# Performance work log

Hardware: AMD Instinct MI355X
Metric: run time of the kernel (lower is better)

Reference implementation:

```python
import jax, jax.numpy as jnp
import numpy as np

B, C, H, W = 8, 512, 64, 64
K = 19       # num classes (Cityscapes)
CT = 256     # transform channels


def _proj(x, w, g, b):
    # 1x1 conv (no bias) + folded eval-mode BatchNorm (per-channel scale g, bias b) + ReLU
    # x: [B,Cin,H,W], w: [Cout,Cin]
    y = jnp.einsum('bchw,oc->bohw', x, w)
    return jax.nn.relu(y * g[None, :, None, None] + b[None, :, None, None])


def setup_inputs() -> dict:
    key = jax.random.key(0)
    ks = jax.random.split(key, 12)
    s = lambda i, shape: jax.random.normal(ks[i], shape, jnp.float32) * 0.05
    ones = lambda n: jnp.ones((n,), jnp.float32)
    zeros = lambda n: jnp.zeros((n,), jnp.float32)
    return {
        'x': jax.random.normal(ks[0], (B, C, H, W), jnp.float32),
        'preds': jax.random.normal(ks[1], (B, K, H, W), jnp.float32),
        'feats_il': jax.random.normal(ks[2], (B, C, H, W), jnp.float32),
        # query_project: two 1x1 conv+BN+ReLU blocks
        'q_w1': s(3, (CT, C)), 'q_g1': ones(CT), 'q_b1': zeros(CT),
        'q_w2': s(4, (CT, CT)), 'q_g2': ones(CT), 'q_b2': zeros(CT),
        # key_project: two 1x1 conv+BN+ReLU blocks
        'k_w1': s(5, (CT, C)), 'k_g1': ones(CT), 'k_b1': zeros(CT),
        'k_w2': s(6, (CT, CT)), 'k_g2': ones(CT), 'k_b2': zeros(CT),
        # value_project: one 1x1 conv+BN+ReLU (value_out_norm=True)
        'v_w': s(7, (CT, C)), 'v_g': ones(CT), 'v_b': zeros(CT),
        # out_project: one 1x1 conv+BN+ReLU
        'o_w': s(8, (C, CT)), 'o_g': ones(C), 'o_b': zeros(C),
    }


def reference(x, preds, feats_il, q_w1, q_g1, q_b1, q_w2, q_g2, q_b2,
              k_w1, k_g1, k_b1, k_w2, k_g2, k_b2, v_w, v_g, v_b, o_w, o_g, o_b):
    b, c, h, w = x.shape
    k = preds.shape[1]
    hw = h * w
    feats = x.reshape(b, c, hw).transpose(0, 2, 1)        # [B,HW,C]
    logits = preds.reshape(b, k, hw).transpose(0, 2, 1)   # [B,HW,K]
    argmax = jnp.argmax(logits, axis=-1)                  # [B,HW]
    onehot = jax.nn.one_hot(argmax, k, dtype=x.dtype)     # [B,HW,K]
    NEG = jnp.asarray(-1e9, x.dtype)
    masked = jnp.where(onehot > 0, logits, NEG)
    # per-class softmax over the pixels assigned to that class
    wgt = jax.nn.softmax(masked, axis=1)                  # [B,HW,K]
    cls_feat = jnp.einsum('bpk,bpc->bkc', wgt, feats)     # [B,K,C]
    # scatter class descriptor back to every pixel of that class
    feats_sl = jnp.take_along_axis(cls_feat, argmax[:, :, None], axis=1)  # [B,HW,C]
    feats_sl = feats_sl.transpose(0, 2, 1).reshape(b, c, h, w)
    # SelfAttentionBlock: query from inputs, key/value from feats_sl
    q = _proj(_proj(x, q_w1, q_g1, q_b1), q_w2, q_g2, q_b2)
    kk = _proj(_proj(feats_sl, k_w1, k_g1, k_b1), k_w2, k_g2, k_b2)
    v = _proj(feats_sl, v_w, v_g, v_b)
    ct = q.shape[1]
    qf = q.reshape(b, ct, hw).transpose(0, 2, 1)          # [B,HW,CT]
    kf = kk.reshape(b, ct, hw)                            # [B,CT,HW]
    vf = v.reshape(b, ct, hw).transpose(0, 2, 1)          # [B,HW,CT]
    sim = jnp.einsum('bqc,bck->bqk', qf, kf) * (ct ** -0.5)
    attn = jax.nn.softmax(sim, axis=-1)
    ctx = jnp.einsum('bqk,bkc->bqc', attn, vf)            # [B,HW,CT]
    ctx = ctx.transpose(0, 2, 1).reshape(b, ct, h, w)
    return _proj(ctx, o_w, o_g, o_b)
```

## Files before the change

### kernel.cpp

```cpp
#include <hip/hip_runtime.h>
#include <math.h>

#define HW 4096
#define NB 8
#define NK 19
#define CIN 512
#define CTC 256

typedef __attribute__((ext_vector_type(8))) short short8;
typedef __attribute__((ext_vector_type(4))) float f32x4;

__device__ inline unsigned short f2bf(float x) {
  unsigned u = __float_as_uint(x);
  return (unsigned short)((u + 0x7fffu + ((u >> 16) & 1u)) >> 16);
}
__device__ inline float bf2f(unsigned short h) {
  return __uint_as_float(((unsigned)h) << 16);
}
__device__ inline void gload16(const void* g, void* l) {
  __builtin_amdgcn_global_load_lds(
      (const __attribute__((address_space(1))) void*)g,
      (__attribute__((address_space(3))) void*)l, 16, 0, 0);
}

__global__ __launch_bounds__(256) void wk1a(
    const float* __restrict__ w1, const float* __restrict__ w2,
    const float* __restrict__ wo, unsigned short* __restrict__ wb1,
    unsigned short* __restrict__ wb2, unsigned short* __restrict__ wbo,
    uint4* __restrict__ cls_feat_z, const float* __restrict__ preds,
    float* __restrict__ bestg, int* __restrict__ clsg,
    unsigned int* __restrict__ Mu_part, unsigned int* __restrict__ cnt_part) {
  __shared__ unsigned int Mw[NK];
  __shared__ unsigned int Cw[NK];
  int bx = blockIdx.x;
  int tid = threadIdx.x;
  if (bx < 320) {
    int gid = bx * 256 + tid;
    int i = gid * 4;
    const float* src;
    unsigned short* dst;
    int off;
    if (i < 131072) { src = w1; dst = wb1; off = i; }
    else if (i < 196608) { src = w2; dst = wb2; off = i - 131072; }
    else { src = wo; dst = wbo; off = i - 196608; }
    float4 v = *(const float4*)(src + off);
    dst[off + 0] = f2bf(v.x);
    dst[off + 1] = f2bf(v.y);
    dst[off + 2] = f2bf(v.z);
    dst[off + 3] = f2bf(v.w);
    uint4 z = {0u, 0u, 0u, 0u};
    for (int j = gid; j < 19456; j += 81920) cls_feat_z[j] = z;
  } else {
    int bq = bx - 320;
    int b = bq >> 4, pblk = bq & 15;
    if (tid < NK) { Mw[tid] = 0u; Cw[tid] = 0u; }
    __syncthreads();
    int p = pblk * 256 + tid;
    const float* pb = preds + (size_t)b * NK * HW;
    float best = pb[p];
    int bi = 0;
#pragma unroll
    for (int k = 1; k < NK; ++k) {
      float v = pb[k * HW + p];
      if (v > best) { best = v; bi = k; }
    }
    bestg[b * HW + p] = best;
    clsg[b * HW + p] = bi;
    unsigned fb = __float_as_uint(best);
    unsigned key = (fb & 0x80000000u) ? ~fb : (fb | 0x80000000u);
    atomicMax(&Mw[bi], key);
    atomicAdd(&Cw[bi], 1u);
    __syncthreads();
    if (tid < 32) {
      Mu_part[(b * 16 + pblk) * 32 + tid] = (tid < NK) ? Mw[tid] : 0u;
      cnt_part[(b * 16 + pblk) * 32 + tid] = (tid < NK) ? Cw[tid] : 0u;
    }
  }
}

__global__ __launch_bounds__(256) void k1b(
    float* __restrict__ bestg, const int* __restrict__ clsg,
    const unsigned int* __restrict__ Mu_part, float* __restrict__ Zf_part) {
  int b = blockIdx.y, pblk = blockIdx.x;
  int tid = threadIdx.x;
  __shared__ float Mf[NK];
  __shared__ float Zw[NK];
  if (tid < NK) {
    unsigned key = 0u;
#pragma unroll
    for (int j = 0; j < 16; ++j) {
      unsigned v = Mu_part[(b * 16 + j) * 32 + tid];
      key = (v > key) ? v : key;
    }
    float m = -1e30f;
    if (key) {
      unsigned fb = (key & 0x80000000u) ? (key & 0x7fffffffu) : ~key;
      m = __uint_as_float(fb);
    }
    Mf[tid] = m;
    Zw[tid] = 0.f;
  }
  __syncthreads();
  int p = pblk * 256 + tid;
  int c = clsg[b * HW + p];
  float e = expf(bestg[b * HW + p] - Mf[c]);
  bestg[b * HW + p] = e;
  atomicAdd(&Zw[c], e);
  __syncthreads();
  if (tid < 32) Zf_part[(b * 16 + pblk) * 32 + tid] = (tid < NK) ? Zw[tid] : 0.f;
}

__global__ __launch_bounds__(256) void xk2(
    const float* __restrict__ x, const float* __restrict__ eg,
    const int* __restrict__ clsg, const float* __restrict__ Zf_part,
    unsigned short* __restrict__ xT, float* __restrict__ cls_feat) {
  __shared__ float tile[64][65];
  __shared__ unsigned short Bs[32 * 516];
  __shared__ float Zl[NK];
  int b = blockIdx.z, c0 = blockIdx.y * 64, pbase = blockIdx.x * 512;
  int tid = threadIdx.x;
  int l = tid & 63, w = tid >> 6;
  if (tid < NK) {
    float s = 0.f;
#pragma unroll
    for (int j = 0; j < 16; ++j) s += Zf_part[(b * 16 + j) * 32 + tid];
    Zl[tid] = s;
  }
  {
    uint4 z = {0u, 0u, 0u, 0u};
    for (int i = tid; i < 2064; i += 256) ((uint4*)Bs)[i] = z;
  }
  __syncthreads();
  for (int i = tid; i < 512; i += 256) {
    int c = clsg[b * HW + pbase + i];
    Bs[c * 516 + i] = f2bf(eg[b * HW + pbase + i] / Zl[c]);
  }
  f32x4 acc[2];
  acc[0] = (f32x4){0.f, 0.f, 0.f, 0.f};
  acc[1] = (f32x4){0.f, 0.f, 0.f, 0.f};
  int cbase = w * 16;
  for (int s = 0; s < 8; ++s) {
    int ps = pbase + s * 64;
    __syncthreads();
#pragma unroll
    for (int r = 0; r < 4; ++r) {
      int cl = r * 16 + (tid >> 4);
      int pl = (tid & 15) * 4;
      float4 v = *(const float4*)&x[((size_t)b * CIN + c0 + cl) * HW + ps + pl];
      tile[cl][pl + 0] = v.x;
      tile[cl][pl + 1] = v.y;
      tile[cl][pl + 2] = v.z;
      tile[cl][pl + 3] = v.w;
    }
    __syncthreads();
#pragma unroll
    for (int j = 0; j < 16; ++j) {
      int ploc = j * 4 + w;
      xT[((size_t)b * HW + ps + ploc) * CIN + c0 + l] = f2bf(tile[l][ploc]);
    }
#pragma unroll
    for (int ch = 0; ch < 2; ++ch) {
      int pt = ch * 32 + (l >> 4) * 8;
      union { short8 v; unsigned short u[8]; } af;
      const float* tp = &tile[cbase + (l & 15)][pt];
#pragma unroll
      for (int j = 0; j < 8; ++j) af.u[j] = f2bf(tp[j]);
      int pg = s * 64 + pt;
#pragma unroll
      for (int mf = 0; mf < 2; ++mf) {
        short8 bf = *(const short8*)&Bs[(mf * 16 + (l & 15)) * 516 + pg];
        acc[mf] =
            __builtin_amdgcn_mfma_f32_16x16x32_bf16(af.v, bf, acc[mf], 0, 0, 0);
      }
    }
  }
#pragma unroll
  for (int mf = 0; mf < 2; ++mf) {
    int k = mf * 16 + (l & 15);
    if (k < NK) {
#pragma unroll
      for (int r = 0; r < 4; ++r) {
        int c = c0 + cbase + (l >> 4) * 4 + r;
        atomicAdd(&cls_feat[((size_t)b * NK + k) * CIN + c], acc[mf][r]);
      }
    }
  }
}

__global__ __launch_bounds__(256) void k3a(
    const float* __restrict__ cls_feat, const float* __restrict__ kw1,
    const float* __restrict__ kg1, const float* __restrict__ kb1,
    const float* __restrict__ vw, const float* __restrict__ vg,
    const float* __restrict__ vb, float* __restrict__ h1g,
    float* __restrict__ Vcls) {
  int bk = blockIdx.y;
  int b = bk / NK, kc = bk % NK;
  int q = blockIdx.x;
  __shared__ float cf[CIN];
  int tid = threadIdx.x;
  const float* row = cls_feat + (size_t)bk * CIN;
  for (int i = tid; i < CIN; i += 256) cf[i] = row[i];
  __syncthreads();
  int o = tid >> 1, half = tid & 1;
  int col = q * 64 + (o & 63);
  const float* w =
      (o < 64) ? &kw1[(size_t)col * CIN] : &vw[(size_t)col * CIN];
  int base = half * 256;
  float acc[4] = {0.f, 0.f, 0.f, 0.f};
#pragma unroll 8
  for (int i = 0; i < 64; ++i) {
    float4 w4 = *(const float4*)&w[base + i * 4];
    const float* c4 = &cf[base + i * 4];
    acc[i & 3] += w4.x * c4[0] + w4.y * c4[1] + w4.z * c4[2] + w4.w * c4[3];
  }
  float s = (acc[0] + acc[1]) + (acc[2] + acc[3]);
  s += __shfl_xor(s, 1);
  if (half == 0) {
    if (o < 64) {
      h1g[(size_t)bk * CTC + col] = fmaxf(s * kg1[col] + kb1[col], 0.f);
    } else {
      Vcls[((size_t)b * CTC + col) * NK + kc] =
          fmaxf(s * vg[col] + vb[col], 0.f);
    }
  }
}

__global__ __launch_bounds__(256) void k3b(
    const float* __restrict__ h1g, const float* __restrict__ kw2,
    const float* __restrict__ kg2, const float* __restrict__ kb2,
    unsigned short* __restrict__ KclsT) {
  int bk = blockIdx.y;
  int q = blockIdx.x;
  __shared__ float h1[CTC];
  int tid = threadIdx.x;
  const float* row = h1g + (size_t)bk * CTC;
  if (tid < CTC) h1[tid] = row[tid];
  __syncthreads();
  int o = tid >> 2, part = tid & 3;
  int col = q * 64 + o;
  const float* w = &kw2[(size_t)col * CTC + part * 64];
  const float* c = &h1[part * 64];
  float acc[4] = {0.f, 0.f, 0.f, 0.f};
#pragma unroll
  for (int i = 0; i < 16; ++i) {
    float4 w4 = *(const float4*)&w[i * 4];
    acc[i & 3] += w4.x * c[i * 4] + w4.y * c[i * 4 + 1] + w4.z * c[i * 4 + 2] +
                  w4.w * c[i * 4 + 3];
  }
  float s = (acc[0] + acc[1]) + (acc[2] + acc[3]);
  s += __shfl_xor(s, 1);
  s += __shfl_xor(s, 2);
  if (part == 0)
    KclsT[(size_t)bk * CTC + col] = f2bf(fmaxf(s * kg2[col] + kb2[col], 0.f));
}

template <int KD>
__global__ __launch_bounds__(256) void gemm_mfma(
    const unsigned short* __restrict__ A, const unsigned short* __restrict__ Wb,
    const float* __restrict__ g, const float* __restrict__ bb,
    void* __restrict__ Y, int M, int outmode) {
  __shared__ __align__(16) unsigned short As[2][128 * 32];
  __shared__ __align__(16) unsigned short Bs[2][128 * 32];
  int b = blockIdx.z;
  int n0 = blockIdx.x * 128;
  int m0 = blockIdx.y * 128;
  int tid = threadIdx.x;
  int l = tid & 63, wid = tid >> 6;
  int wr = wid >> 1, wc = wid & 1;
  const unsigned short* Ab = A + (size_t)b * HW * KD;

  f32x4 acc[4][4];
#pragma unroll
  for (int i = 0; i < 4; ++i)
#pragma unroll
    for (int j = 0; j < 4; ++j) acc[i][j] = (f32x4){0.f, 0.f, 0.f, 0.f};

  const int NT = KD / 32;
  auto STAGE = [&](int buf, int t) {
    int k0 = t * 32;
#pragma unroll
    for (int q = 0; q < 2; ++q) {
      int e = q * 2048 + tid * 8;
      int rl = e >> 5, sl = (e >> 3) & 3;
      gload16(Ab + (size_t)(n0 + rl) * KD + k0 + 8 * (sl ^ ((rl >> 1) & 3)),
              &As[buf][q * 2048 + wid * 512]);
    }
#pragma unroll
    for (int q = 0; q < 2; ++q) {
      int e = q * 2048 + tid * 8;
      int rl = e >> 5, sl = (e >> 3) & 3;
      gload16(Wb + (size_t)(m0 + rl) * KD + k0 + 8 * (sl ^ ((rl >> 1) & 3)),
              &Bs[buf][q * 2048 + wid * 512]);
    }
  };
  STAGE(0, 0);
  for (int t = 0; t < NT; ++t) {
    __syncthreads();
    if (t + 1 < NT) STAGE((t + 1) & 1, t + 1);
    int cur = t & 1;
    short8 af[4], bf[4];
#pragma unroll
    for (int f = 0; f < 4; ++f) {
      int nl = wr * 64 + f * 16 + (l & 15);
      af[f] = *(const short8*)&As[cur][nl * 32 + 8 * ((l >> 4) ^ ((nl >> 1) & 3))];
      int ml = wc * 64 + f * 16 + (l & 15);
      bf[f] = *(const short8*)&Bs[cur][ml * 32 + 8 * ((l >> 4) ^ ((ml >> 1) & 3))];
    }
#pragma unroll
    for (int i = 0; i < 4; ++i)
#pragma unroll
      for (int j = 0; j < 4; ++j)
        acc[i][j] =
            __builtin_amdgcn_mfma_f32_16x16x32_bf16(af[i], bf[j], acc[i][j], 0, 0, 0);
  }
  if (outmode == 0) {
    float* Yf = (float*)Y + (size_t)b * M * HW;
#pragma unroll
    for (int j = 0; j < 4; ++j) {
      int m = m0 + wc * 64 + j * 16 + (l & 15);
      float gm = g[m], bm = bb[m];
#pragma unroll
      for (int i = 0; i < 4; ++i) {
        int n = n0 + wr * 64 + i * 16 + (l >> 4) * 4;
        float4 o;
        o.x = fmaxf(acc[i][j][0] * gm + bm, 0.f);
        o.y = fmaxf(acc[i][j][1] * gm + bm, 0.f);
        o.z = fmaxf(acc[i][j][2] * gm + bm, 0.f);
        o.w = fmaxf(acc[i][j][3] * gm + bm, 0.f);
        *(float4*)&Yf[(size_t)m * HW + n] = o;
      }
    }
  } else {
    unsigned short* Yt = (unsigned short*)Y + (size_t)b * HW * M;
#pragma unroll
    for (int j = 0; j < 4; ++j) {
      int m = m0 + wc * 64 + j * 16 + (l & 15);
      float gm = g[m], bm = bb[m];
#pragma unroll
      for (int i = 0; i < 4; ++i) {
        int n = n0 + wr * 64 + i * 16 + (l >> 4) * 4;
#pragma unroll
        for (int r = 0; r < 4; ++r)
          Yt[(size_t)(n + r) * M + m] = f2bf(fmaxf(acc[i][j][r] * gm + bm, 0.f));
      }
    }
  }
}

__global__ __launch_bounds__(256, 1) void g1g2k5(
    const unsigned short* __restrict__ xT, const unsigned short* __restrict__ W1,
    const float* __restrict__ g1, const float* __restrict__ b1,
    const unsigned short* __restrict__ W2, const float* __restrict__ g2,
    const float* __restrict__ b2, const unsigned short* __restrict__ KclsT,
    const float* __restrict__ Vcls, const unsigned int* __restrict__ cnt_part,
    unsigned short* __restrict__ ctxT) {
  __shared__ __align__(16) char RC[49152];
  __shared__ __align__(16) unsigned short Q1f[8][4096];
  __shared__ __align__(16) unsigned short Kl2[32 * 32 * 8];
  __shared__ __align__(16) unsigned short Vl2[4 * 256 * 8];
  __shared__ float cntl[NK];
  unsigned short* As = (unsigned short*)RC;
  unsigned short* Bs = (unsigned short*)(RC + 16384);
  float* simT = (float*)RC;
  unsigned short* Pl = (unsigned short*)(RC + 16896);

  int b = blockIdx.y;
  int p0 = blockIdx.x * 128;
  int tid = threadIdx.x;
  int l = tid & 63, w = tid >> 6;
  const unsigned short* xTb = xT + ((size_t)b * HW + p0) * CIN;

  for (int i = tid; i < NK * 32; i += 256) {
    int m = i >> 5, s = i & 31;
    short8 v = *(const short8*)&KclsT[((size_t)b * NK + m) * CTC + s * 8];
    *(short8*)&Kl2[(s * 32 + m) * 8] = v;
  }
  for (int i = tid; i < 4 * 256; i += 256) {
    int s = i >> 8, c = i & 255;
    union { short8 v; unsigned short u[8]; } pk;
    const float* vr = &Vcls[((size_t)b * CTC + c) * NK];
#pragma unroll
    for (int j = 0; j < 8; ++j) {
      int k = s * 8 + j;
      pk.u[j] = (k < NK) ? f2bf(vr[k]) : (unsigned short)0;
    }
    *(short8*)&Vl2[(s * 256 + c) * 8] = pk.v;
  }
  if (tid < NK) {
    unsigned int s = 0u;
#pragma unroll
    for (int j = 0; j < 16; ++j) s += cnt_part[(b * 16 + j) * 32 + tid];
    cntl[tid] = (float)s;
  }

  f32x4 acc[2][16];

  auto STAGE_A1 = [&](int buf, int t) {
    int k0 = t * 32;
#pragma unroll
    for (int q = 0; q < 2; ++q) {
      int e = q * 2048 + tid * 8;
      int rl = e >> 5, sl = (e >> 3) & 3;
      gload16(xTb + (size_t)rl * CIN + k0 + 8 * (sl ^ ((rl >> 1) & 3)),
              &As[buf * 4096 + q * 2048 + w * 512]);
    }
  };
  auto STAGE_B1 = [&](int buf, int t) {
    int k0 = t * 32;
#pragma unroll
    for (int q = 0; q < 4; ++q) {
      int e = q * 2048 + tid * 8;
      int rl = e >> 5, sl = (e >> 3) & 3;
      gload16(W1 + (size_t)rl * CIN + k0 + 8 * (sl ^ ((rl >> 1) & 3)),
              &Bs[buf * 8192 + q * 2048 + w * 512]);
    }
  };
#pragma unroll
  for (int i = 0; i < 2; ++i)
#pragma unroll
    for (int j = 0; j < 16; ++j) acc[i][j] = (f32x4){0.f, 0.f, 0.f, 0.f};
  STAGE_A1(0, 0);
  STAGE_B1(0, 0);
  for (int t = 0; t < 16; ++t) {
    __syncthreads();
    if (t + 1 < 16) { STAGE_A1((t + 1) & 1, t + 1); STAGE_B1((t + 1) & 1, t + 1); }
    int cur = t & 1;
    short8 af[2];
#pragma unroll
    for (int f = 0; f < 2; ++f) {
      int nl = w * 32 + f * 16 + (l & 15);
      af[f] =
          *(const short8*)&As[cur * 4096 + nl * 32 + 8 * ((l >> 4) ^ ((nl >> 1) & 3))];
    }
#pragma unroll
    for (int mf = 0; mf < 16; ++mf) {
      int ml = mf * 16 + (l & 15);
      short8 bf =
          *(const short8*)&Bs[cur * 8192 + ml * 32 + 8 * ((l >> 4) ^ ((ml >> 1) & 3))];
      acc[0][mf] =
          __builtin_amdgcn_mfma_f32_16x16x32_bf16(af[0], bf, acc[0][mf], 0, 0, 0);
      acc[1][mf] =
          __builtin_amdgcn_mfma_f32_16x16x32_bf16(af[1], bf, acc[1][mf], 0, 0, 0);
    }
  }
#pragma unroll
  for (int mf = 0; mf < 16; ++mf) {
    int ch = mf * 16 + (l & 15);
    float gm = g1[ch], bm = b1[ch];
    int tq = ch >> 5, slot = (ch >> 3) & 3, wi = ch & 7;
#pragma unroll
    for (int i = 0; i < 2; ++i) {
#pragma unroll
      for (int r = 0; r < 4; ++r) {
        int p = w * 32 + i * 16 + (l >> 4) * 4 + r;
        Q1f[tq][p * 32 + 8 * (slot ^ ((p >> 1) & 3)) + wi] =
            f2bf(fmaxf(acc[i][mf][r] * gm + bm, 0.f));
      }
    }
  }

  auto STAGE_B2 = [&](int buf, int t) {
    int k0 = t * 32;
#pragma unroll
    for (int q = 0; q < 4; ++q) {
      int e = q * 2048 + tid * 8;
      int rl = e >> 5, sl = (e >> 3) & 3;
      gload16(W2 + (size_t)rl * CTC + k0 + 8 * (sl ^ ((rl >> 1) & 3)),
              &Bs[buf * 8192 + q * 2048 + w * 512]);
    }
  };
#pragma unroll
  for (int i = 0; i < 2; ++i)
#pragma unroll
    for (int j = 0; j < 16; ++j) acc[i][j] = (f32x4){0.f, 0.f, 0.f, 0.f};
  STAGE_B2(0, 0);
  for (int t = 0; t < 8; ++t) {
    __syncthreads();
    if (t + 1 < 8) STAGE_B2((t + 1) & 1, t + 1);
    int cur = t & 1;
    short8 af[2];
#pragma unroll
    for (int f = 0; f < 2; ++f) {
      int nl = w * 32 + f * 16 + (l & 15);
      af[f] = *(const short8*)&Q1f[t][nl * 32 + 8 * ((l >> 4) ^ ((nl >> 1) & 3))];
    }
#pragma unroll
    for (int mf = 0; mf < 16; ++mf) {
      int ml = mf * 16 + (l & 15);
      short8 bf =
          *(const short8*)&Bs[cur * 8192 + ml * 32 + 8 * ((l >> 4) ^ ((ml >> 1) & 3))];
      acc[0][mf] =
          __builtin_amdgcn_mfma_f32_16x16x32_bf16(af[0], bf, acc[0][mf], 0, 0, 0);
      acc[1][mf] =
          __builtin_amdgcn_mfma_f32_16x16x32_bf16(af[1], bf, acc[1][mf], 0, 0, 0);
    }
  }
  __syncthreads();
#pragma unroll
  for (int mf = 0; mf < 16; ++mf) {
    int ch = mf * 16 + (l & 15);
    float gm = g2[ch], bm = b2[ch];
    int tq = ch >> 5, slot = (ch >> 3) & 3, wi = ch & 7;
#pragma unroll
    for (int i = 0; i < 2; ++i) {
#pragma unroll
      for (int r = 0; r < 4; ++r) {
        int p = w * 32 + i * 16 + (l >> 4) * 4 + r;
        Q1f[tq][p * 32 + 8 * (slot ^ ((p >> 1) & 3)) + wi] =
            f2bf(fmaxf(acc[i][mf][r] * gm + bm, 0.f));
      }
    }
  }
  __syncthreads();

  f32x4 a2[2][2];
#pragma unroll
  for (int i = 0; i < 2; ++i)
#pragma unroll
    for (int j = 0; j < 2; ++j) a2[i][j] = (f32x4){0.f, 0.f, 0.f, 0.f};
  for (int t = 0; t < 8; ++t) {
    short8 aq[2], bk[2];
#pragma unroll
    for (int f = 0; f < 2; ++f) {
      int nl = w * 32 + f * 16 + (l & 15);
      aq[f] = *(const short8*)&Q1f[t][nl * 32 + 8 * ((l >> 4) ^ ((nl >> 1) & 3))];
      int s = t * 4 + (l >> 4);
      int ml = f * 16 + (l & 15);
      bk[f] = *(const short8*)&Kl2[(s * 32 + ml) * 8];
    }
#pragma unroll
    for (int i = 0; i < 2; ++i)
#pragma unroll
      for (int j = 0; j < 2; ++j)
        a2[i][j] =
            __builtin_amdgcn_mfma_f32_16x16x32_bf16(aq[i], bk[j], a2[i][j], 0, 0, 0);
  }
  __syncthreads();
#pragma unroll
  for (int i = 0; i < 2; ++i)
#pragma unroll
    for (int j = 0; j < 2; ++j) {
      int m = j * 16 + (l & 15);
      if (m < NK) {
#pragma unroll
        for (int r = 0; r < 4; ++r) {
          int p = w * 32 + i * 16 + (l >> 4) * 4 + r;
          simT[p * 33 + m] = a2[i][j][r];
        }
      }
    }
  __syncthreads();
  if (tid < 128) {
    float sims[NK];
#pragma unroll
    for (int k = 0; k < NK; ++k) sims[k] = simT[tid * 33 + k] * 0.0625f;
    float m = -1e30f;
#pragma unroll
    for (int k = 0; k < NK; ++k)
      if (cntl[k] > 0.f) m = fmaxf(m, sims[k]);
    float d = 0.f;
#pragma unroll
    for (int k = 0; k < NK; ++k) {
      float e = (cntl[k] > 0.f) ? expf(sims[k] - m) : 0.f;
      sims[k] = cntl[k] * e;
      d += sims[k];
    }
    float inv = 1.f / d;
#pragma unroll
    for (int s = 0; s < 4; ++s) {
      union { short8 v; unsigned short u8[8]; } pk;
#pragma unroll
      for (int j = 0; j < 8; ++j) {
        int k = s * 8 + j;
        pk.u8[j] = (k < NK) ? f2bf(sims[k] * inv) : (unsigned short)0;
      }
      *(short8*)&Pl[(s * 128 + tid) * 8] = pk.v;
    }
  }
  __syncthreads();
  short8 ap[2];
#pragma unroll
  for (int f = 0; f < 2; ++f) {
    int nl = w * 32 + f * 16 + (l & 15);
    ap[f] = *(const short8*)&Pl[((l >> 4) * 128 + nl) * 8];
  }
  unsigned short* cb = ctxT + ((size_t)b * HW + p0) * CTC;
#pragma unroll
  for (int mc = 0; mc < 4; ++mc) {
#pragma unroll
    for (int mf = 0; mf < 4; ++mf) {
      int ml = mc * 64 + mf * 16 + (l & 15);
      short8 bv = *(const short8*)&Vl2[((l >> 4) * 256 + ml) * 8];
#pragma unroll
      for (int nf = 0; nf < 2; ++nf) {
        f32x4 z = {0.f, 0.f, 0.f, 0.f};
        f32x4 o = __builtin_amdgcn_mfma_f32_16x16x32_bf16(ap[nf], bv, z, 0, 0, 0);
#pragma unroll
        for (int r = 0; r < 4; ++r) {
          int p = w * 32 + nf * 16 + (l >> 4) * 4 + r;
          cb[(size_t)p * CTC + ml] = f2bf(o[r]);
        }
      }
    }
  }
}

extern "C" void kernel_launch(void* const* d_in, const int* in_sizes, int n_in,
                              void* d_out, int out_size, void* d_ws, size_t ws_size,
                              hipStream_t stream) {
  const float* x = (const float*)d_in[0];
  const float* preds = (const float*)d_in[1];
  const float* q_w1 = (const float*)d_in[3];
  const float* q_g1 = (const float*)d_in[4];
  const float* q_b1 = (const float*)d_in[5];
  const float* q_w2 = (const float*)d_in[6];
  const float* q_g2 = (const float*)d_in[7];
  const float* q_b2 = (const float*)d_in[8];
  const float* k_w1 = (const float*)d_in[9];
  const float* k_g1 = (const float*)d_in[10];
  const float* k_b1 = (const float*)d_in[11];
  const float* k_w2 = (const float*)d_in[12];
  const float* k_g2 = (const float*)d_in[13];
  const float* k_b2 = (const float*)d_in[14];
  const float* v_w = (const float*)d_in[15];
  const float* v_g = (const float*)d_in[16];
  const float* v_b = (const float*)d_in[17];
  const float* o_w = (const float*)d_in[18];
  const float* o_g = (const float*)d_in[19];
  const float* o_b = (const float*)d_in[20];
  float* out = (float*)d_out;

  char* base = (char*)d_ws;
  unsigned short* xT = (unsigned short*)base;
  unsigned short* ctxT = (unsigned short*)(base + 33554432);
  char* f32r = base + 50331648;
  float* cls_feat = (float*)f32r;
  unsigned short* KclsT = (unsigned short*)(f32r + 311296);
  float* Vcls = (float*)(f32r + 389120);
  unsigned short* wb1 = (unsigned short*)(f32r + 544768);
  unsigned short* wb2 = (unsigned short*)(f32r + 806912);
  unsigned short* wbo = (unsigned short*)(f32r + 937984);
  float* h1g = (float*)(f32r + 1200128);
  float* bestg = (float*)(f32r + 1355776);
  int* clsg = (int*)(f32r + 1486848);
  unsigned int* Mu_part = (unsigned int*)(f32r + 1617920);
  unsigned int* cnt_part = (unsigned int*)(f32r + 1634304);
  float* Zf_part = (float*)(f32r + 1650688);

  wk1a<<<448, 256, 0, stream>>>(q_w1, q_w2, o_w, wb1, wb2, wbo,
                                (uint4*)cls_feat, preds, bestg, clsg, Mu_part,
                                cnt_part);
  k1b<<<dim3(16, NB), 256, 0, stream>>>(bestg, clsg, Mu_part, Zf_part);
  xk2<<<dim3(8, 8, NB), 256, 0, stream>>>(x, bestg, clsg, Zf_part, xT,
                                          cls_feat);
  k3a<<<dim3(4, NB * NK), 256, 0, stream>>>(cls_feat, k_w1, k_g1, k_b1, v_w,
                                            v_g, v_b, h1g, Vcls);
  k3b<<<dim3(4, NB * NK), 256, 0, stream>>>(h1g, k_w2, k_g2, k_b2, KclsT);
  g1g2k5<<<dim3(HW / 128, NB), 256, 0, stream>>>(xT, wb1, q_g1, q_b1, wb2,
                                                 q_g2, q_b2, KclsT, Vcls,
                                                 cnt_part, ctxT);
  gemm_mfma<CTC><<<dim3(32, 4, NB), 256, 0, stream>>>(ctxT, wbo, o_g, o_b,
                                                      (void*)out, CIN, 0);
}
```

Baseline: 128.8 us.

## Double fused query-attention kernel to 512 threads with a 4x2 wave split

The fused Q-projection/attention kernel now runs with 8 waves instead of 4. In the two GEMM phases each wave covers 32 pixels by 128 channels rather than 32 by 256, which halves per-wave accumulator registers. In the attention phase each wave handles 16 pixels instead of 32. The aim is more latency hiding and MFMA issue parallelism per CU with the same shared-memory footprint, at the cost of more barrier participants and duplicated A-fragment loads across waves.

New measurement: 119.1 us. 7.5% less time.

```diff
diff --git a/kernel.cpp b/kernel.cpp
--- a/kernel.cpp
+++ b/kernel.cpp
@@ -347,7 +347,7 @@
   }
 }
 
-__global__ __launch_bounds__(256, 1) void g1g2k5(
+__global__ __launch_bounds__(512, 1) void g1g2k5(
     const unsigned short* __restrict__ xT, const unsigned short* __restrict__ W1,
     const float* __restrict__ g1, const float* __restrict__ b1,
     const unsigned short* __restrict__ W2, const float* __restrict__ g2,
@@ -368,14 +368,15 @@
   int p0 = blockIdx.x * 128;
   int tid = threadIdx.x;
   int l = tid & 63, w = tid >> 6;
+  int wp = w & 3, wm = w >> 2;
   const unsigned short* xTb = xT + ((size_t)b * HW + p0) * CIN;
 
-  for (int i = tid; i < NK * 32; i += 256) {
+  for (int i = tid; i < NK * 32; i += 512) {
     int m = i >> 5, s = i & 31;
     short8 v = *(const short8*)&KclsT[((size_t)b * NK + m) * CTC + s * 8];
     *(short8*)&Kl2[(s * 32 + m) * 8] = v;
   }
-  for (int i = tid; i < 4 * 256; i += 256) {
+  for (int i = tid; i < 4 * 256; i += 512) {
     int s = i >> 8, c = i & 255;
     union { short8 v; unsigned short u[8]; } pk;
     const float* vr = &Vcls[((size_t)b * CTC + c) * NK];
@@ -393,32 +394,29 @@
     cntl[tid] = (float)s;
   }
 
-  f32x4 acc[2][16];
+  f32x4 acc[2][8];
 
   auto STAGE_A1 = [&](int buf, int t) {
     int k0 = t * 32;
-#pragma unroll
-    for (int q = 0; q < 2; ++q) {
-      int e = q * 2048 + tid * 8;
-      int rl = e >> 5, sl = (e >> 3) & 3;
-      gload16(xTb + (size_t)rl * CIN + k0 + 8 * (sl ^ ((rl >> 1) & 3)),
-              &As[buf * 4096 + q * 2048 + w * 512]);
-    }
+    int e = tid * 8;
+    int rl = e >> 5, sl = (e >> 3) & 3;
+    gload16(xTb + (size_t)rl * CIN + k0 + 8 * (sl ^ ((rl >> 1) & 3)),
+            &As[buf * 4096 + w * 512]);
   };
   auto STAGE_B1 = [&](int buf, int t) {
     int k0 = t * 32;
 #pragma unroll
-    for (int q = 0; q < 4; ++q) {
-      int e = q * 2048 + tid * 8;
+    for (int q = 0; q < 2; ++q) {
+      int e = q * 4096 + tid * 8;
       int rl = e >> 5, sl = (e >> 3) & 3;
       gload16(W1 + (size_t)rl * CIN + k0 + 8 * (sl ^ ((rl >> 1) & 3)),
-              &Bs[buf * 8192 + q * 2048 + w * 512]);
+              &Bs[buf * 8192 + q * 4096 + w * 512]);
     }
   };
 #pragma unroll
   for (int i = 0; i < 2; ++i)
 #pragma unroll
-    for (int j = 0; j < 16; ++j) acc[i][j] = (f32x4){0.f, 0.f, 0.f, 0.f};
+    for (int j = 0; j < 8; ++j) acc[i][j] = (f32x4){0.f, 0.f, 0.f, 0.f};
   STAGE_A1(0, 0);
   STAGE_B1(0, 0);
   for (int t = 0; t < 16; ++t) {
@@ -428,13 +426,13 @@
     short8 af[2];
 #pragma unroll
     for (int f = 0; f < 2; ++f) {
-      int nl = w * 32 + f * 16 + (l & 15);
+      int nl = wp * 32 + f * 16 + (l & 15);
       af[f] =
           *(const short8*)&As[cur * 4096 + nl * 32 + 8 * ((l >> 4) ^ ((nl >> 1) & 3))];
     }
 #pragma unroll
-    for (int mf = 0; mf < 16; ++mf) {
-      int ml = mf * 16 + (l & 15);
+    for (int mf = 0; mf < 8; ++mf) {
+      int ml = wm * 128 + mf * 16 + (l & 15);
       short8 bf =
           *(const short8*)&Bs[cur * 8192 + ml * 32 + 8 * ((l >> 4) ^ ((ml >> 1) & 3))];
       acc[0][mf] =
@@ -444,15 +442,15 @@
     }
   }
 #pragma unroll
-  for (int mf = 0; mf < 16; ++mf) {
-    int ch = mf * 16 + (l & 15);
+  for (int mf = 0; mf < 8; ++mf) {
+    int ch = wm * 128 + mf * 16 + (l & 15);
     float gm = g1[ch], bm = b1[ch];
     int tq = ch >> 5, slot = (ch >> 3) & 3, wi = ch & 7;
 #pragma unroll
     for (int i = 0; i < 2; ++i) {
 #pragma unroll
       for (int r = 0; r < 4; ++r) {
-        int p = w * 32 + i * 16 + (l >> 4) * 4 + r;
+        int p = wp * 32 + i * 16 + (l >> 4) * 4 + r;
         Q1f[tq][p * 32 + 8 * (slot ^ ((p >> 1) & 3)) + wi] =
             f2bf(fmaxf(acc[i][mf][r] * gm + bm, 0.f));
       }
@@ -462,17 +460,17 @@
   auto STAGE_B2 = [&](int buf, int t) {
     int k0 = t * 32;
 #pragma unroll
-    for (int q = 0; q < 4; ++q) {
-      int e = q * 2048 + tid * 8;
+    for (int q = 0; q < 2; ++q) {
+      int e = q * 4096 + tid * 8;
       int rl = e >> 5, sl = (e >> 3) & 3;
       gload16(W2 + (size_t)rl * CTC + k0 + 8 * (sl ^ ((rl >> 1) & 3)),
-              &Bs[buf * 8192 + q * 2048 + w * 512]);
+              &Bs[buf * 8192 + q * 4096 + w * 512]);
     }
   };
 #pragma unroll
   for (int i = 0; i < 2; ++i)
 #pragma unroll
-    for (int j = 0; j < 16; ++j) acc[i][j] = (f32x4){0.f, 0.f, 0.f, 0.f};
+    for (int j = 0; j < 8; ++j) acc[i][j] = (f32x4){0.f, 0.f, 0.f, 0.f};
   STAGE_B2(0, 0);
   for (int t = 0; t < 8; ++t) {
     __syncthreads();
@@ -481,12 +479,12 @@
     short8 af[2];
 #pragma unroll
     for (int f = 0; f < 2; ++f) {
-      int nl = w * 32 + f * 16 + (l & 15);
+      int nl = wp * 32 + f * 16 + (l & 15);
       af[f] = *(const short8*)&Q1f[t][nl * 32 + 8 * ((l >> 4) ^ ((nl >> 1) & 3))];
     }
 #pragma unroll
-    for (int mf = 0; mf < 16; ++mf) {
-      int ml = mf * 16 + (l & 15);
+    for (int mf = 0; mf < 8; ++mf) {
+      int ml = wm * 128 + mf * 16 + (l & 15);
       short8 bf =
           *(const short8*)&Bs[cur * 8192 + ml * 32 + 8 * ((l >> 4) ^ ((ml >> 1) & 3))];
       acc[0][mf] =
@@ -497,15 +495,15 @@
   }
   __syncthreads();
 #pragma unroll
-  for (int mf = 0; mf < 16; ++mf) {
-    int ch = mf * 16 + (l & 15);
+  for (int mf = 0; mf < 8; ++mf) {
+    int ch = wm * 128 + mf * 16 + (l & 15);
     float gm = g2[ch], bm = b2[ch];
     int tq = ch >> 5, slot = (ch >> 3) & 3, wi = ch & 7;
 #pragma unroll
     for (int i = 0; i < 2; ++i) {
 #pragma unroll
       for (int r = 0; r < 4; ++r) {
-        int p = w * 32 + i * 16 + (l >> 4) * 4 + r;
+        int p = wp * 32 + i * 16 + (l >> 4) * 4 + r;
         Q1f[tq][p * 32 + 8 * (slot ^ ((p >> 1) & 3)) + wi] =
             f2bf(fmaxf(acc[i][mf][r] * gm + bm, 0.f));
       }
@@ -513,42 +511,33 @@
   }
   __syncthreads();
 
-  f32x4 a2[2][2];
-#pragma unroll
-  for (int i = 0; i < 2; ++i)
-#pragma unroll
-    for (int j = 0; j < 2; ++j) a2[i][j] = (f32x4){0.f, 0.f, 0.f, 0.f};
+  f32x4 a2[2];
+  a2[0] = (f32x4){0.f, 0.f, 0.f, 0.f};
+  a2[1] = (f32x4){0.f, 0.f, 0.f, 0.f};
   for (int t = 0; t < 8; ++t) {
-    short8 aq[2], bk[2];
-#pragma unroll
-    for (int f = 0; f < 2; ++f) {
-      int nl = w * 32 + f * 16 + (l & 15);
-      aq[f] = *(const short8*)&Q1f[t][nl * 32 + 8 * ((l >> 4) ^ ((nl >> 1) & 3))];
-      int s = t * 4 + (l >> 4);
-      int ml = f * 16 + (l & 15);
-      bk[f] = *(const short8*)&Kl2[(s * 32 + ml) * 8];
-    }
-#pragma unroll
-    for (int i = 0; i < 2; ++i)
-#pragma unroll
-      for (int j = 0; j < 2; ++j)
-        a2[i][j] =
-            __builtin_amdgcn_mfma_f32_16x16x32_bf16(aq[i], bk[j], a2[i][j], 0, 0, 0);
-  }
-  __syncthreads();
-#pragma unroll
-  for (int i = 0; i < 2; ++i)
+    int nl = w * 16 + (l & 15);
+    short8 aq =
+        *(const short8*)&Q1f[t][nl * 32 + 8 * ((l >> 4) ^ ((nl >> 1) & 3))];
+    int s = t * 4 + (l >> 4);
 #pragma unroll
     for (int j = 0; j < 2; ++j) {
-      int m = j * 16 + (l & 15);
-      if (m < NK) {
-#pragma unroll
-        for (int r = 0; r < 4; ++r) {
-          int p = w * 32 + i * 16 + (l >> 4) * 4 + r;
-          simT[p * 33 + m] = a2[i][j][r];
-        }
-      }
-    }
+      int ml = j * 16 + (l & 15);
+      short8 bk = *(const short8*)&Kl2[(s * 32 + ml) * 8];
+      a2[j] = __builtin_amdgcn_mfma_f32_16x16x32_bf16(aq, bk, a2[j], 0, 0, 0);
+    }
+  }
+  __syncthreads();
+#pragma unroll
+  for (int j = 0; j < 2; ++j) {
+    int m = j * 16 + (l & 15);
+    if (m < NK) {
+#pragma unroll
+      for (int r = 0; r < 4; ++r) {
+        int p = w * 16 + (l >> 4) * 4 + r;
+        simT[p * 33 + m] = a2[j][r];
+      }
+    }
+  }
   __syncthreads();
   if (tid < 128) {
     float sims[NK];
@@ -578,11 +567,10 @@
     }
   }
   __syncthreads();
-  short8 ap[2];
-#pragma unroll
-  for (int f = 0; f < 2; ++f) {
-    int nl = w * 32 + f * 16 + (l & 15);
-    ap[f] = *(const short8*)&Pl[((l >> 4) * 128 + nl) * 8];
+  short8 ap;
+  {
+    int nl = w * 16 + (l & 15);
+    ap = *(const short8*)&Pl[((l >> 4) * 128 + nl) * 8];
   }
   unsigned short* cb = ctxT + ((size_t)b * HW + p0) * CTC;
 #pragma unroll
@@ -591,15 +579,12 @@
     for (int mf = 0; mf < 4; ++mf) {
       int ml = mc * 64 + mf * 16 + (l & 15);
       short8 bv = *(const short8*)&Vl2[((l >> 4) * 256 + ml) * 8];
-#pragma unroll
-      for (int nf = 0; nf < 2; ++nf) {
-        f32x4 z = {0.f, 0.f, 0.f, 0.f};
-        f32x4 o = __builtin_amdgcn_mfma_f32_16x16x32_bf16(ap[nf], bv, z, 0, 0, 0);
-#pragma unroll
-        for (int r = 0; r < 4; ++r) {
-          int p = w * 32 + nf * 16 + (l >> 4) * 4 + r;
-          cb[(size_t)p * CTC + ml] = f2bf(o[r]);
-        }
+      f32x4 z = {0.f, 0.f, 0.f, 0.f};
+      f32x4 o = __builtin_amdgcn_mfma_f32_16x16x32_bf16(ap, bv, z, 0, 0, 0);
+#pragma unroll
+      for (int r = 0; r < 4; ++r) {
+        int p = w * 16 + (l >> 4) * 4 + r;
+        cb[(size_t)p * CTC + ml] = f2bf(o[r]);
       }
     }
   }
@@ -656,7 +641,7 @@
   k3a<<<dim3(4, NB * NK), 256, 0, stream>>>(cls_feat, k_w1, k_g1, k_b1, v_w,
                                             v_g, v_b, h1g, Vcls);
   k3b<<<dim3(4, NB * NK), 256, 0, stream>>>(h1g, k_w2, k_g2, k_b2, KclsT);
-  g1g2k5<<<dim3(HW / 128, NB), 256, 0, stream>>>(xT, wb1, q_g1, q_b1, wb2,
+  g1g2k5<<<dim3(HW / 128, NB), 512, 0, stream>>>(xT, wb1, q_g1, q_b1, wb2,
                                                  q_g2, q_b2, KclsT, Vcls,
                                                  cnt_part, ctxT);
   gemm_mfma<CTC><<<dim3(32, 4, NB), 256, 0, stream>>>(ctxT, wbo, o_g, o_b,
```
